# Kernel optimization log

Hardware: AMD Instinct MI355X
Metric: run time of the kernel (lower is better)

The kernel has to match this reference:

```python
import jax, jax.numpy as jnp
import numpy as np

N_NODES = 100_000
N_EDGES = 1_600_000
D = 128
BN_EPS = 1e-5
GIN_EPS = 0.0  # GINConv default eps, train_eps=False


def setup_inputs() -> dict:
    key = jax.random.key(0)
    ks = jax.random.split(key, 8)
    x = jax.random.normal(ks[0], (N_NODES, D), dtype=jnp.float32)
    edge_index = jax.random.randint(ks[1], (2, N_EDGES), 0, N_NODES, dtype=jnp.int64)
    s = 1.0 / np.sqrt(D)
    W1 = jax.random.uniform(ks[2], (D, D), jnp.float32, -s, s)
    b1 = jax.random.uniform(ks[3], (D,), jnp.float32, -s, s)
    W2 = jax.random.uniform(ks[4], (D, D), jnp.float32, -s, s)
    b2 = jax.random.uniform(ks[5], (D,), jnp.float32, -s, s)
    W3 = jax.random.uniform(ks[6], (D, D), jnp.float32, -s, s)
    g1 = jnp.ones((D,), jnp.float32)
    be1 = jnp.zeros((D,), jnp.float32)
    g2 = jnp.ones((D,), jnp.float32)
    be2 = jnp.zeros((D,), jnp.float32)
    return {"x": x, "edge_index": edge_index,
            "W1": W1, "b1": b1, "g1": g1, "be1": be1,
            "W2": W2, "b2": b2, "g2": g2, "be2": be2,
            "W3": W3}


def _batchnorm(h, gamma, beta):
    # training-mode BatchNorm1d over node dim with biased variance
    mean = jnp.mean(h, axis=0)
    var = jnp.mean(jnp.square(h - mean), axis=0)
    return (h - mean) * jax.lax.rsqrt(var + BN_EPS) * gamma + beta


def reference(x, edge_index, W1, b1, g1, be1, W2, b2, g2, be2, W3):
    src, dst = edge_index[0], edge_index[1]
    # GIN aggregation: (1+eps)*x_i + sum_{j->i} x_j  (scatter-add over edges)
    agg = jax.ops.segment_sum(x[src], dst, num_segments=N_NODES)
    h = (1.0 + GIN_EPS) * x + agg
    # MLP: Linear+BN+ReLU x2, then Linear (no bias)
    h = jax.nn.relu(_batchnorm(h @ W1.T + b1, g1, be1))
    h = jax.nn.relu(_batchnorm(h @ W2.T + b2, g2, be2))
    h = h @ W3.T
    # GINLayer final activation (bn=None)
    return jax.nn.relu(h)
```

## Files before the change

### kernel.cpp

```cpp
#include <hip/hip_runtime.h>

#define NN 100000
#define NE 1600000
#define DD 128
#define NCB 196
#define TILE 2048
#define NTILE 782
#define TILEC 4096
#define NTILEC 391
#define FCAP 12288
#define SREP 32
#define WPAD 17408
#define GROWS 256

typedef __attribute__((ext_vector_type(8))) short bf16x8;
typedef __attribute__((ext_vector_type(4))) float f32x4;

union u4bf8 { uint4 u; bf16x8 v; };

__device__ __forceinline__ ushort f2bf(float f) {
    union { float f; uint i; } v; v.f = f;
    uint i = v.i;
    return (ushort)((i + 0x7fffu + ((i >> 16) & 1u)) >> 16);
}
__device__ __forceinline__ float bf2f(ushort u) {
    union { uint i; float f; } v; v.i = ((uint)u) << 16; return v.f;
}
__device__ __forceinline__ float blo(uint v) { return bf2f((ushort)(v & 0xffffu)); }
__device__ __forceinline__ float bhi(uint v) { return bf2f((ushort)(v >> 16)); }

__global__ __launch_bounds__(256) void k_xbh(const float* __restrict__ x,
                                             uint* __restrict__ xb,
                                             const int* __restrict__ ei,
                                             int* __restrict__ ghistP,
                                             const float* __restrict__ W1,
                                             const float* __restrict__ W2,
                                             const float* __restrict__ W3,
                                             ushort* __restrict__ Wbp) {
    __shared__ int h[NCB];
    int t = threadIdx.x;
    if (t < NCB) h[t] = 0;
    __syncthreads();
    int base = blockIdx.x * TILE;
#pragma unroll
    for (int i = 0; i < 8; ++i) {
        int e = base + i * 256 + t;
        if (e < NE) atomicAdd(&h[ei[NE + e] >> 9], 1);
    }
    int gid = blockIdx.x * 256 + t;
#pragma unroll
    for (int i = 0; i < 8; ++i) {
        int item = i * (NTILE * 256) + gid;
        if (item < NN * 16) {
            int n = item >> 4, q = item & 15;
            const float* xp = x + (size_t)n * DD + q * 8;
            float4 a = *(const float4*)xp;
            float4 b = *(const float4*)(xp + 4);
            uint4 pk;
            pk.x = (uint)f2bf(a.x) | ((uint)f2bf(a.y) << 16);
            pk.y = (uint)f2bf(a.z) | ((uint)f2bf(a.w) << 16);
            pk.z = (uint)f2bf(b.x) | ((uint)f2bf(b.y) << 16);
            pk.w = (uint)f2bf(b.z) | ((uint)f2bf(b.w) << 16);
            *(uint4*)(xb + (size_t)n * 64 + q * 4) = pk;
        }
    }
    int c = gid;
    if (c < 6144) {
        int l = c >> 11;
        int cc = c & 2047;
        int r = cc >> 4, c8 = (cc & 15) * 8;
        const float* Wl = (l == 0) ? W1 : (l == 1) ? W2 : W3;
        const float* p = Wl + r * DD + c8;
        float4 a = *(const float4*)p;
        float4 b = *(const float4*)(p + 4);
        uint4 pk;
        pk.x = (uint)f2bf(a.x) | ((uint)f2bf(a.y) << 16);
        pk.y = (uint)f2bf(a.z) | ((uint)f2bf(a.w) << 16);
        pk.z = (uint)f2bf(b.x) | ((uint)f2bf(b.y) << 16);
        pk.w = (uint)f2bf(b.z) | ((uint)f2bf(b.w) << 16);
        *(uint4*)&Wbp[(size_t)l * WPAD + r * 136 + c8] = pk;
    }
    __syncthreads();
    if (t < NCB && h[t] > 0) atomicAdd(&ghistP[t * 16], h[t]);
}

__global__ __launch_bounds__(256) void k_cscatter(const int* __restrict__ ei,
                                                  const int* __restrict__ ghistP,
                                                  int* __restrict__ gcurP,
                                                  uint* __restrict__ buck) {
    __shared__ int h[NCB];
    __shared__ int tb[NCB];
    __shared__ int sh[256];
    int t = threadIdx.x;
    if (t < NCB) h[t] = 0;
    __syncthreads();
    int base = blockIdx.x * TILEC;
    uint vv[16]; int bb[16]; int rr[16];
#pragma unroll
    for (int i = 0; i < 16; ++i) {
        int e = base + i * 256 + t;
        bb[i] = -1;
        if (e < NE) {
            int s = ei[e], d = ei[NE + e];
            int b = d >> 9;
            bb[i] = b;
            vv[i] = (uint)s | ((uint)(d & 511) << 17);
            rr[i] = atomicAdd(&h[b], 1);
        }
    }
    __syncthreads();
    int my = (t < NCB) ? ghistP[t * 16] : 0;
    sh[t] = my;
    __syncthreads();
    for (int o = 1; o < 256; o <<= 1) {
        int u = (t >= o) ? sh[t - o] : 0;
        __syncthreads();
        sh[t] += u;
        __syncthreads();
    }
    if (t < NCB && h[t] > 0)
        tb[t] = (sh[t] - my) + atomicAdd(&gcurP[t * 16], h[t]);
    __syncthreads();
#pragma unroll
    for (int i = 0; i < 16; ++i) {
        if (bb[i] >= 0) buck[tb[bb[i]] + rr[i]] = vv[i];
    }
}

__global__ __launch_bounds__(256) void k_fsort(const uint* __restrict__ buck,
                                               const int* __restrict__ ghistP,
                                               int* __restrict__ csr,
                                               int* __restrict__ rowp) {
    __shared__ uint ebuf[FCAP];
    __shared__ int cnt[512];
    __shared__ int sd[256];
    __shared__ int sh[256];
    int c = blockIdx.x, t = threadIdx.x;
    cnt[t] = 0; cnt[t + 256] = 0;
    int my = (t < NCB) ? ghistP[t * 16] : 0;
    sh[t] = my;
    __syncthreads();
    for (int o = 1; o < 256; o <<= 1) {
        int u = (t >= o) ? sh[t - o] : 0;
        __syncthreads();
        sh[t] += u;
        __syncthreads();
    }
    int s1 = sh[c];
    int hc = ghistP[c * 16];
    int s0 = s1 - hc;
    int len = hc;
    int cap = (len < FCAP) ? len : FCAP;
    for (int i = t; i < cap; i += 256) ebuf[i] = buck[s0 + i];
    __syncthreads();
    for (int i = t; i < len; i += 256) {
        uint v = (i < FCAP) ? ebuf[i] : buck[s0 + i];
        atomicAdd(&cnt[(v >> 17) & 511], 1);
    }
    __syncthreads();
    int p = cnt[2 * t], q = cnt[2 * t + 1];
    sd[t] = p + q;
    __syncthreads();
    for (int o = 1; o < 256; o <<= 1) {
        int u = (t >= o) ? sd[t - o] : 0;
        __syncthreads();
        sd[t] += u;
        __syncthreads();
    }
    int base = sd[t] - (p + q);
    rowp[c * 512 + 2 * t]     = s0 + base;
    rowp[c * 512 + 2 * t + 1] = s0 + base + p;
    __syncthreads();
    cnt[2 * t] = base;
    cnt[2 * t + 1] = base + p;
    __syncthreads();
    for (int i = t; i < len; i += 256) {
        uint v = (i < FCAP) ? ebuf[i] : buck[s0 + i];
        int ld = (int)((v >> 17) & 511u);
        int pos = atomicAdd(&cnt[ld], 1);
        csr[s0 + pos] = (int)(v & 0x1FFFFu);
    }
}

#define B8(ACC0, ACC1, SJ, J)                                               \
    {                                                                       \
        int s0 = __shfl(SJ, J),     s1 = __shfl(SJ, J + 1);                 \
        int s2 = __shfl(SJ, J + 2), s3 = __shfl(SJ, J + 3);                 \
        int s4 = __shfl(SJ, J + 4), s5 = __shfl(SJ, J + 5);                 \
        int s6 = __shfl(SJ, J + 6), s7 = __shfl(SJ, J + 7);                 \
        uint v0 = xb[(size_t)s0 * 64 + lane], v1 = xb[(size_t)s1 * 64 + lane]; \
        uint v2 = xb[(size_t)s2 * 64 + lane], v3 = xb[(size_t)s3 * 64 + lane]; \
        uint v4 = xb[(size_t)s4 * 64 + lane], v5 = xb[(size_t)s5 * 64 + lane]; \
        uint v6 = xb[(size_t)s6 * 64 + lane], v7 = xb[(size_t)s7 * 64 + lane]; \
        ACC0 += blo(v0) + blo(v1) + blo(v2) + blo(v3)                       \
              + blo(v4) + blo(v5) + blo(v6) + blo(v7);                      \
        ACC1 += bhi(v0) + bhi(v1) + bhi(v2) + bhi(v3)                       \
              + bhi(v4) + bhi(v5) + bhi(v6) + bhi(v7);                      \
    }

__global__ __launch_bounds__(256) void k_gather(const uint* __restrict__ xb,
                                                const int* __restrict__ rowp,
                                                const int* __restrict__ csr,
                                                ushort* __restrict__ agg) {
    const int HALF = NN / 2;
    int wave = threadIdx.x >> 6, lane = threadIdx.x & 63;
    int w = blockIdx.x * 4 + wave;
    if (w >= HALF) return;
    int nA = w, nB = w + HALF;
    uint sA = xb[(size_t)nA * 64 + lane];
    uint sB = xb[(size_t)nB * 64 + lane];
    float a0 = blo(sA), a1 = bhi(sA);
    float b0 = blo(sB), b1 = bhi(sB);
    int iA = rowp[nA], eA = rowp[nA + 1];
    int iB = rowp[nB], eB = rowp[nB + 1];

    while (iA < eA || iB < eB) {
        int mA = eA - iA; if (mA > 64) mA = 64; if (mA < 0) mA = 0;
        int mB = eB - iB; if (mB > 64) mB = 64; if (mB < 0) mB = 0;
        int sjA = (lane < mA) ? csr[iA + lane] : 0;
        int sjB = (lane < mB) ? csr[iB + lane] : 0;
        int j = 0, k = 0;
        while (j + 8 <= mA && k + 8 <= mB) {
            int t0 = __shfl(sjA, j),     t1 = __shfl(sjA, j + 1);
            int t2 = __shfl(sjA, j + 2), t3 = __shfl(sjA, j + 3);
            int t4 = __shfl(sjA, j + 4), t5 = __shfl(sjA, j + 5);
            int t6 = __shfl(sjA, j + 6), t7 = __shfl(sjA, j + 7);
            int u0 = __shfl(sjB, k),     u1 = __shfl(sjB, k + 1);
            int u2 = __shfl(sjB, k + 2), u3 = __shfl(sjB, k + 3);
            int u4 = __shfl(sjB, k + 4), u5 = __shfl(sjB, k + 5);
            int u6 = __shfl(sjB, k + 6), u7 = __shfl(sjB, k + 7);
            uint vA0 = xb[(size_t)t0 * 64 + lane], vA1 = xb[(size_t)t1 * 64 + lane];
            uint vA2 = xb[(size_t)t2 * 64 + lane], vA3 = xb[(size_t)t3 * 64 + lane];
            uint vA4 = xb[(size_t)t4 * 64 + lane], vA5 = xb[(size_t)t5 * 64 + lane];
            uint vA6 = xb[(size_t)t6 * 64 + lane], vA7 = xb[(size_t)t7 * 64 + lane];
            uint vB0 = xb[(size_t)u0 * 64 + lane], vB1 = xb[(size_t)u1 * 64 + lane];
            uint vB2 = xb[(size_t)u2 * 64 + lane], vB3 = xb[(size_t)u3 * 64 + lane];
            uint vB4 = xb[(size_t)u4 * 64 + lane], vB5 = xb[(size_t)u5 * 64 + lane];
            uint vB6 = xb[(size_t)u6 * 64 + lane], vB7 = xb[(size_t)u7 * 64 + lane];
            a0 += blo(vA0) + blo(vA1) + blo(vA2) + blo(vA3)
                + blo(vA4) + blo(vA5) + blo(vA6) + blo(vA7);
            a1 += bhi(vA0) + bhi(vA1) + bhi(vA2) + bhi(vA3)
                + bhi(vA4) + bhi(vA5) + bhi(vA6) + bhi(vA7);
            b0 += blo(vB0) + blo(vB1) + blo(vB2) + blo(vB3)
                + blo(vB4) + blo(vB5) + blo(vB6) + blo(vB7);
            b1 += bhi(vB0) + bhi(vB1) + bhi(vB2) + bhi(vB3)
                + bhi(vB4) + bhi(vB5) + bhi(vB6) + bhi(vB7);
            j += 8; k += 8;
        }
        while (j + 8 <= mA) { B8(a0, a1, sjA, j) j += 8; }
        while (k + 8 <= mB) { B8(b0, b1, sjB, k) k += 8; }
        while (j < mA && k < mB) {
            int t = __shfl(sjA, j); int u = __shfl(sjB, k);
            uint vA = xb[(size_t)t * 64 + lane];
            uint vB = xb[(size_t)u * 64 + lane];
            a0 += blo(vA); a1 += bhi(vA);
            b0 += blo(vB); b1 += bhi(vB);
            ++j; ++k;
        }
        while (j < mA) {
            int t = __shfl(sjA, j++);
            uint vA = xb[(size_t)t * 64 + lane];
            a0 += blo(vA); a1 += bhi(vA);
        }
        while (k < mB) {
            int u = __shfl(sjB, k++);
            uint vB = xb[(size_t)u * 64 + lane];
            b0 += blo(vB); b1 += bhi(vB);
        }
        iA += mA; iB += mB;
    }

    uint pkA = (uint)f2bf(a0) | ((uint)f2bf(a1) << 16);
    uint pkB = (uint)f2bf(b0) | ((uint)f2bf(b1) << 16);
    ((uint*)(agg + (size_t)nA * DD))[lane] = pkA;
    ((uint*)(agg + (size_t)nB * DD))[lane] = pkB;
}

template <int MODE>
__global__ __launch_bounds__(256) void k_gemm(const ushort* __restrict__ Ain,
                                              const ushort* __restrict__ Wp,
                                              const float* __restrict__ bias,
                                              const float* __restrict__ statsIn,
                                              const float* __restrict__ g,
                                              const float* __restrict__ be,
                                              void* __restrict__ Outv,
                                              float* __restrict__ statsOut) {
    __shared__ __align__(16) ushort lw[DD * 136];
    __shared__ float red[2][4][DD];
    __shared__ float lac[2 * DD];

    int tid = threadIdx.x;
    int wave = tid >> 6, lane = tid & 63;
    int lm = lane & 15, quad = lane >> 4;

    int row00 = blockIdx.x * GROWS + wave * 16;
    int ar0 = (row00 + lm < NN) ? row00 + lm : 0;
    uint4 araw[4];
#pragma unroll
    for (int kb = 0; kb < 4; ++kb) {
        araw[kb] = *(const uint4*)(Ain + (size_t)ar0 * DD + kb * 32 + quad * 8);
    }

#pragma unroll
    for (int it = 0; it < 8; ++it) {
        int o8 = (it * 256 + tid) * 8;
        *(uint4*)&lw[o8] = *(const uint4*)&Wp[o8];
    }
    if (tid < 128) {
        int o8 = 16384 + tid * 8;
        *(uint4*)&lw[o8] = *(const uint4*)&Wp[o8];
    }
    if constexpr (MODE != 1) {
        if (tid < DD) {
            float S = 0.f, Q = 0.f;
#pragma unroll
            for (int r = 0; r < SREP; ++r) {
                S += statsIn[(r << 8) + tid];
                Q += statsIn[(r << 8) + DD + tid];
            }
            float inv = 1.f / (float)NN;
            float mean = S * inv;
            float var = Q * inv - mean * mean;
            float a = g[tid] * rsqrtf(var + 1e-5f);
            lac[tid] = a;
            lac[DD + tid] = be[tid] - mean * a;
        }
    }
    __syncthreads();

    ushort* Out16 = (ushort*)Outv;
    float* Out32 = (float*)Outv;

    float csum[8], csq[8];
#pragma unroll
    for (int nt = 0; nt < 8; ++nt) { csum[nt] = 0.f; csq[nt] = 0.f; }

#pragma unroll
    for (int sub = 0; sub < 4; ++sub) {
        int row0 = blockIdx.x * GROWS + sub * 64 + wave * 16;
        int arow = row0 + lm;
        int ar = (arow < NN) ? arow : 0;

        bf16x8 afrag[4];
#pragma unroll
        for (int kb = 0; kb < 4; ++kb) {
            int k0 = kb * 32 + quad * 8;
            u4bf8 u;
            if (sub == 0) u.u = araw[kb];
            else          u.u = *(const uint4*)(Ain + (size_t)ar * DD + k0);
            if constexpr (MODE == 1) {
                afrag[kb] = u.v;
            } else {
                uint pk[4] = {u.u.x, u.u.y, u.u.z, u.u.w};
                bf16x8 af;
#pragma unroll
                for (int jj = 0; jj < 4; ++jj) {
                    int k = k0 + jj * 2;
                    float v0 = blo(pk[jj]);
                    float v1 = bhi(pk[jj]);
                    v0 = fmaxf(fmaf(v0, lac[k], lac[DD + k]), 0.f);
                    v1 = fmaxf(fmaf(v1, lac[k + 1], lac[DD + k + 1]), 0.f);
                    af[jj * 2]     = (short)f2bf(v0);
                    af[jj * 2 + 1] = (short)f2bf(v1);
                }
                afrag[kb] = af;
            }
        }

        f32x4 acc[8];
#pragma unroll
        for (int nt = 0; nt < 8; ++nt) {
            float bv = (MODE == 3) ? 0.f : bias[nt * 16 + lm];
            acc[nt] = (f32x4){bv, bv, bv, bv};
        }

#pragma unroll
        for (int kb = 0; kb < 4; ++kb) {
#pragma unroll
            for (int nt = 0; nt < 8; ++nt) {
                bf16x8 bfrag = *(const bf16x8*)&lw[(nt * 16 + lm) * 136 + kb * 32 + quad * 8];
                acc[nt] = __builtin_amdgcn_mfma_f32_16x16x32_bf16(afrag[kb], bfrag, acc[nt], 0, 0, 0);
            }
        }

#pragma unroll
        for (int nt = 0; nt < 8; ++nt) {
            int col = nt * 16 + lm;
#pragma unroll
            for (int r = 0; r < 4; ++r) {
                int row = row0 + quad * 4 + r;
                float v = acc[nt][r];
                if (MODE == 3) v = fmaxf(v, 0.f);
                if (row < NN) {
                    if constexpr (MODE == 3) Out32[(size_t)row * DD + col] = v;
                    else Out16[(size_t)row * DD + col] = f2bf(v);
                    csum[nt] += v;
                    csq[nt] += v * v;
                }
            }
        }
    }

    if constexpr (MODE != 3) {
#pragma unroll
        for (int nt = 0; nt < 8; ++nt) {
            float s = csum[nt], q = csq[nt];
            s += __shfl_down(s, 16, 64); q += __shfl_down(q, 16, 64);
            s += __shfl_down(s, 32, 64); q += __shfl_down(q, 32, 64);
            if (quad == 0) {
                red[0][wave][nt * 16 + lm] = s;
                red[1][wave][nt * 16 + lm] = q;
            }
        }
        __syncthreads();
        if (tid < DD) {
            float S = red[0][0][tid] + red[0][1][tid] + red[0][2][tid] + red[0][3][tid];
            float Q = red[1][0][tid] + red[1][1][tid] + red[1][2][tid] + red[1][3][tid];
            int rep = (blockIdx.x & (SREP - 1)) << 8;
            atomicAdd(&statsOut[rep + tid], S);
            atomicAdd(&statsOut[rep + DD + tid], Q);
        }
    }
}

extern "C" void kernel_launch(void* const* d_in, const int* in_sizes, int n_in,
                              void* d_out, int out_size, void* d_ws, size_t ws_size,
                              hipStream_t stream) {
    const float* x   = (const float*)d_in[0];
    const int* ei    = (const int*)d_in[1];
    const float* W1  = (const float*)d_in[2];
    const float* b1  = (const float*)d_in[3];
    const float* g1  = (const float*)d_in[4];
    const float* be1 = (const float*)d_in[5];
    const float* W2  = (const float*)d_in[6];
    const float* b2  = (const float*)d_in[7];
    const float* g2  = (const float*)d_in[8];
    const float* be2 = (const float*)d_in[9];
    const float* W3  = (const float*)d_in[10];

    float* stats  = (float*)d_ws;
    float* stats2 = stats + SREP * 256;
    int* ghistP   = (int*)(stats2 + SREP * 256);
    int* gcurP    = ghistP + NCB * 16;
    ushort* Wbp   = (ushort*)(gcurP + NCB * 16);
    int* rowp     = (int*)(Wbp + 3 * WPAD);
    uint* buck    = (uint*)(rowp + NCB * 512 + 4);
    int* csr      = (int*)(buck + NE);
    ushort* agg   = (ushort*)(((uintptr_t)(csr + NE) + 15) & ~(uintptr_t)15);
    uint* xb     = (uint*)d_out;
    ushort* t1   = (ushort*)d_out + (size_t)NN * DD;
    ushort* t2   = agg;
    float* outp  = (float*)d_out;

    int gblk = (NN + GROWS - 1) / GROWS;
    hipMemsetAsync(stats, 0, (2 * SREP * 256) * sizeof(float) + 2 * NCB * 16 * sizeof(int), stream);
    k_xbh<<<NTILE, 256, 0, stream>>>(x, xb, ei, ghistP, W1, W2, W3, Wbp);
    k_cscatter<<<NTILEC, 256, 0, stream>>>(ei, ghistP, gcurP, buck);
    k_fsort<<<NCB, 256, 0, stream>>>(buck, ghistP, csr, rowp);
    k_gather<<<(NN / 2 + 3) / 4, 256, 0, stream>>>(xb, rowp, csr, agg);
    k_gemm<1><<<gblk, 256, 0, stream>>>(agg, Wbp, b1, nullptr, nullptr, nullptr, t1, stats);
    k_gemm<2><<<gblk, 256, 0, stream>>>(t1, Wbp + WPAD, b2, stats, g1, be1, t2, stats2);
    k_gemm<3><<<gblk, 256, 0, stream>>>(t2, Wbp + 2 * WPAD, nullptr, stats2, g2, be2, outp, nullptr);
}
```

Before: 292.9 us.

## Fuse gather and three GEMM stages into one cooperative persistent kernel

Merges the neighbor-gather kernel and the three MFMA GEMM/BatchNorm stages into a single cooperative kernel. The stages are separated by grid-wide syncs, and the grid is sized from the occupancy query, capped at four blocks per CU. Each stage uses grid-stride loops over its work items. This is meant to remove the launch and drain gaps between the four back-to-back kernels. In exchange it adds grid-sync overhead and caps the gather phase's wave count, which can hurt a latency-bound gather. It also ties the gather phase to the GEMM's LDS footprint.

```diff
diff --git a/kernel.cpp b/kernel.cpp
--- a/kernel.cpp
+++ b/kernel.cpp
@@ -1,4 +1,7 @@
 #include <hip/hip_runtime.h>
+#include <hip/hip_cooperative_groups.h>
+
+namespace cg = cooperative_groups;
 
 #define NN 100000
 #define NE 1600000
@@ -12,6 +15,7 @@
 #define SREP 32
 #define WPAD 17408
 #define GROWS 256
+#define GBLK 391
 
 typedef __attribute__((ext_vector_type(8))) short bf16x8;
 typedef __attribute__((ext_vector_type(4))) float f32x4;
@@ -198,229 +202,254 @@
               + bhi(v4) + bhi(v5) + bhi(v6) + bhi(v7);                      \
     }
 
-__global__ __launch_bounds__(256) void k_gather(const uint* __restrict__ xb,
-                                                const int* __restrict__ rowp,
-                                                const int* __restrict__ csr,
-                                                ushort* __restrict__ agg) {
-    const int HALF = NN / 2;
-    int wave = threadIdx.x >> 6, lane = threadIdx.x & 63;
-    int w = blockIdx.x * 4 + wave;
-    if (w >= HALF) return;
-    int nA = w, nB = w + HALF;
-    uint sA = xb[(size_t)nA * 64 + lane];
-    uint sB = xb[(size_t)nB * 64 + lane];
-    float a0 = blo(sA), a1 = bhi(sA);
-    float b0 = blo(sB), b1 = bhi(sB);
-    int iA = rowp[nA], eA = rowp[nA + 1];
-    int iB = rowp[nB], eB = rowp[nB + 1];
-
-    while (iA < eA || iB < eB) {
-        int mA = eA - iA; if (mA > 64) mA = 64; if (mA < 0) mA = 0;
-        int mB = eB - iB; if (mB > 64) mB = 64; if (mB < 0) mB = 0;
-        int sjA = (lane < mA) ? csr[iA + lane] : 0;
-        int sjB = (lane < mB) ? csr[iB + lane] : 0;
-        int j = 0, k = 0;
-        while (j + 8 <= mA && k + 8 <= mB) {
-            int t0 = __shfl(sjA, j),     t1 = __shfl(sjA, j + 1);
-            int t2 = __shfl(sjA, j + 2), t3 = __shfl(sjA, j + 3);
-            int t4 = __shfl(sjA, j + 4), t5 = __shfl(sjA, j + 5);
-            int t6 = __shfl(sjA, j + 6), t7 = __shfl(sjA, j + 7);
-            int u0 = __shfl(sjB, k),     u1 = __shfl(sjB, k + 1);
-            int u2 = __shfl(sjB, k + 2), u3 = __shfl(sjB, k + 3);
-            int u4 = __shfl(sjB, k + 4), u5 = __shfl(sjB, k + 5);
-            int u6 = __shfl(sjB, k + 6), u7 = __shfl(sjB, k + 7);
-            uint vA0 = xb[(size_t)t0 * 64 + lane], vA1 = xb[(size_t)t1 * 64 + lane];
-            uint vA2 = xb[(size_t)t2 * 64 + lane], vA3 = xb[(size_t)t3 * 64 + lane];
-            uint vA4 = xb[(size_t)t4 * 64 + lane], vA5 = xb[(size_t)t5 * 64 + lane];
-            uint vA6 = xb[(size_t)t6 * 64 + lane], vA7 = xb[(size_t)t7 * 64 + lane];
-            uint vB0 = xb[(size_t)u0 * 64 + lane], vB1 = xb[(size_t)u1 * 64 + lane];
-            uint vB2 = xb[(size_t)u2 * 64 + lane], vB3 = xb[(size_t)u3 * 64 + lane];
-            uint vB4 = xb[(size_t)u4 * 64 + lane], vB5 = xb[(size_t)u5 * 64 + lane];
-            uint vB6 = xb[(size_t)u6 * 64 + lane], vB7 = xb[(size_t)u7 * 64 + lane];
-            a0 += blo(vA0) + blo(vA1) + blo(vA2) + blo(vA3)
-                + blo(vA4) + blo(vA5) + blo(vA6) + blo(vA7);
-            a1 += bhi(vA0) + bhi(vA1) + bhi(vA2) + bhi(vA3)
-                + bhi(vA4) + bhi(vA5) + bhi(vA6) + bhi(vA7);
-            b0 += blo(vB0) + blo(vB1) + blo(vB2) + blo(vB3)
-                + blo(vB4) + blo(vB5) + blo(vB6) + blo(vB7);
-            b1 += bhi(vB0) + bhi(vB1) + bhi(vB2) + bhi(vB3)
-                + bhi(vB4) + bhi(vB5) + bhi(vB6) + bhi(vB7);
-            j += 8; k += 8;
-        }
-        while (j + 8 <= mA) { B8(a0, a1, sjA, j) j += 8; }
-        while (k + 8 <= mB) { B8(b0, b1, sjB, k) k += 8; }
-        while (j < mA && k < mB) {
-            int t = __shfl(sjA, j); int u = __shfl(sjB, k);
-            uint vA = xb[(size_t)t * 64 + lane];
-            uint vB = xb[(size_t)u * 64 + lane];
-            a0 += blo(vA); a1 += bhi(vA);
-            b0 += blo(vB); b1 += bhi(vB);
-            ++j; ++k;
-        }
-        while (j < mA) {
-            int t = __shfl(sjA, j++);
-            uint vA = xb[(size_t)t * 64 + lane];
-            a0 += blo(vA); a1 += bhi(vA);
-        }
-        while (k < mB) {
-            int u = __shfl(sjB, k++);
-            uint vB = xb[(size_t)u * 64 + lane];
-            b0 += blo(vB); b1 += bhi(vB);
-        }
-        iA += mA; iB += mB;
-    }
-
-    uint pkA = (uint)f2bf(a0) | ((uint)f2bf(a1) << 16);
-    uint pkB = (uint)f2bf(b0) | ((uint)f2bf(b1) << 16);
-    ((uint*)(agg + (size_t)nA * DD))[lane] = pkA;
-    ((uint*)(agg + (size_t)nB * DD))[lane] = pkB;
-}
-
 template <int MODE>
-__global__ __launch_bounds__(256) void k_gemm(const ushort* __restrict__ Ain,
-                                              const ushort* __restrict__ Wp,
-                                              const float* __restrict__ bias,
-                                              const float* __restrict__ statsIn,
-                                              const float* __restrict__ g,
-                                              const float* __restrict__ be,
-                                              void* __restrict__ Outv,
-                                              float* __restrict__ statsOut) {
+__device__ void gemm_phase(const ushort* __restrict__ Ain,
+                           const ushort* __restrict__ Wp,
+                           const float* __restrict__ bias,
+                           const float* __restrict__ statsIn,
+                           const float* __restrict__ g,
+                           const float* __restrict__ be,
+                           void* __restrict__ Outv,
+                           float* __restrict__ statsOut,
+                           ushort* lw, float (*red)[4][DD], float* lac) {
+    int tid = threadIdx.x;
+    int wave = tid >> 6, lane = tid & 63;
+    int lm = lane & 15, quad = lane >> 4;
+    ushort* Out16 = (ushort*)Outv;
+    float* Out32 = (float*)Outv;
+
+    for (int tile = blockIdx.x; tile < GBLK; tile += gridDim.x) {
+        int row00 = tile * GROWS + wave * 16;
+        int ar0 = (row00 + lm < NN) ? row00 + lm : 0;
+        uint4 araw[4];
+#pragma unroll
+        for (int kb = 0; kb < 4; ++kb)
+            araw[kb] = *(const uint4*)(Ain + (size_t)ar0 * DD + kb * 32 + quad * 8);
+
+#pragma unroll
+        for (int it = 0; it < 8; ++it) {
+            int o8 = (it * 256 + tid) * 8;
+            *(uint4*)&lw[o8] = *(const uint4*)&Wp[o8];
+        }
+        if (tid < 128) {
+            int o8 = 16384 + tid * 8;
+            *(uint4*)&lw[o8] = *(const uint4*)&Wp[o8];
+        }
+        if constexpr (MODE != 1) {
+            if (tid < DD) {
+                float S = 0.f, Q = 0.f;
+#pragma unroll
+                for (int r = 0; r < SREP; ++r) {
+                    S += statsIn[(r << 8) + tid];
+                    Q += statsIn[(r << 8) + DD + tid];
+                }
+                float inv = 1.f / (float)NN;
+                float mean = S * inv;
+                float var = Q * inv - mean * mean;
+                float a = g[tid] * rsqrtf(var + 1e-5f);
+                lac[tid] = a;
+                lac[DD + tid] = be[tid] - mean * a;
+            }
+        }
+        __syncthreads();
+
+        float csum[8], csq[8];
+#pragma unroll
+        for (int nt = 0; nt < 8; ++nt) { csum[nt] = 0.f; csq[nt] = 0.f; }
+
+#pragma unroll
+        for (int sub = 0; sub < 4; ++sub) {
+            int row0 = tile * GROWS + sub * 64 + wave * 16;
+            int arow = row0 + lm;
+            int ar = (arow < NN) ? arow : 0;
+
+            bf16x8 afrag[4];
+#pragma unroll
+            for (int kb = 0; kb < 4; ++kb) {
+                int k0 = kb * 32 + quad * 8;
+                u4bf8 u;
+                if (sub == 0) u.u = araw[kb];
+                else          u.u = *(const uint4*)(Ain + (size_t)ar * DD + k0);
+                if constexpr (MODE == 1) {
+                    afrag[kb] = u.v;
+                } else {
+                    uint pk[4] = {u.u.x, u.u.y, u.u.z, u.u.w};
+                    bf16x8 af;
+#pragma unroll
+                    for (int jj = 0; jj < 4; ++jj) {
+                        int k = k0 + jj * 2;
+                        float v0 = blo(pk[jj]);
+                        float v1 = bhi(pk[jj]);
+                        v0 = fmaxf(fmaf(v0, lac[k], lac[DD + k]), 0.f);
+                        v1 = fmaxf(fmaf(v1, lac[k + 1], lac[DD + k + 1]), 0.f);
+                        af[jj * 2]     = (short)f2bf(v0);
+                        af[jj * 2 + 1] = (short)f2bf(v1);
+                    }
+                    afrag[kb] = af;
+                }
+            }
+
+            f32x4 acc[8];
+#pragma unroll
+            for (int nt = 0; nt < 8; ++nt) {
+                float bv = (MODE == 3) ? 0.f : bias[nt * 16 + lm];
+                acc[nt] = (f32x4){bv, bv, bv, bv};
+            }
+
+#pragma unroll
+            for (int kb = 0; kb < 4; ++kb) {
+#pragma unroll
+                for (int nt = 0; nt < 8; ++nt) {
+                    bf16x8 bfrag = *(const bf16x8*)&lw[(nt * 16 + lm) * 136 + kb * 32 + quad * 8];
+                    acc[nt] = __builtin_amdgcn_mfma_f32_16x16x32_bf16(afrag[kb], bfrag, acc[nt], 0, 0, 0);
+                }
+            }
+
+#pragma unroll
+            for (int nt = 0; nt < 8; ++nt) {
+                int col = nt * 16 + lm;
+#pragma unroll
+                for (int r = 0; r < 4; ++r) {
+                    int row = row0 + quad * 4 + r;
+                    float v = acc[nt][r];
+                    if (MODE == 3) v = fmaxf(v, 0.f);
+                    if (row < NN) {
+                        if constexpr (MODE == 3) Out32[(size_t)row * DD + col] = v;
+                        else Out16[(size_t)row * DD + col] = f2bf(v);
+                        csum[nt] += v;
+                        csq[nt] += v * v;
+                    }
+                }
+            }
+        }
+
+        if constexpr (MODE != 3) {
+#pragma unroll
+            for (int nt = 0; nt < 8; ++nt) {
+                float s = csum[nt], q = csq[nt];
+                s += __shfl_down(s, 16, 64); q += __shfl_down(q, 16, 64);
+                s += __shfl_down(s, 32, 64); q += __shfl_down(q, 32, 64);
+                if (quad == 0) {
+                    red[0][wave][nt * 16 + lm] = s;
+                    red[1][wave][nt * 16 + lm] = q;
+                }
+            }
+            __syncthreads();
+            if (tid < DD) {
+                float S = red[0][0][tid] + red[0][1][tid] + red[0][2][tid] + red[0][3][tid];
+                float Q = red[1][0][tid] + red[1][1][tid] + red[1][2][tid] + red[1][3][tid];
+                int rep = (tile & (SREP - 1)) << 8;
+                atomicAdd(&statsOut[rep + tid], S);
+                atomicAdd(&statsOut[rep + DD + tid], Q);
+            }
+        }
+        __syncthreads();
+    }
+}
+
+struct TailArgs {
+    const uint* xb; const int* rowp; const int* csr; ushort* agg;
+    const ushort* Wbp;
+    const float* b1; const float* b2;
+    const float* g1; const float* be1; const float* g2; const float* be2;
+    ushort* t1; ushort* t2; float* outp;
+    float* stats; float* stats2;
+};
+
+__global__ __launch_bounds__(256, 4) void k_tail(TailArgs a) {
     __shared__ __align__(16) ushort lw[DD * 136];
     __shared__ float red[2][4][DD];
     __shared__ float lac[2 * DD];
-
-    int tid = threadIdx.x;
-    int wave = tid >> 6, lane = tid & 63;
-    int lm = lane & 15, quad = lane >> 4;
-
-    int row00 = blockIdx.x * GROWS + wave * 16;
-    int ar0 = (row00 + lm < NN) ? row00 + lm : 0;
-    uint4 araw[4];
-#pragma unroll
-    for (int kb = 0; kb < 4; ++kb) {
-        araw[kb] = *(const uint4*)(Ain + (size_t)ar0 * DD + kb * 32 + quad * 8);
-    }
-
-#pragma unroll
-    for (int it = 0; it < 8; ++it) {
-        int o8 = (it * 256 + tid) * 8;
-        *(uint4*)&lw[o8] = *(const uint4*)&Wp[o8];
-    }
-    if (tid < 128) {
-        int o8 = 16384 + tid * 8;
-        *(uint4*)&lw[o8] = *(const uint4*)&Wp[o8];
-    }
-    if constexpr (MODE != 1) {
-        if (tid < DD) {
-            float S = 0.f, Q = 0.f;
-#pragma unroll
-            for (int r = 0; r < SREP; ++r) {
-                S += statsIn[(r << 8) + tid];
-                Q += statsIn[(r << 8) + DD + tid];
-            }
-            float inv = 1.f / (float)NN;
-            float mean = S * inv;
-            float var = Q * inv - mean * mean;
-            float a = g[tid] * rsqrtf(var + 1e-5f);
-            lac[tid] = a;
-            lac[DD + tid] = be[tid] - mean * a;
-        }
-    }
-    __syncthreads();
-
-    ushort* Out16 = (ushort*)Outv;
-    float* Out32 = (float*)Outv;
-
-    float csum[8], csq[8];
-#pragma unroll
-    for (int nt = 0; nt < 8; ++nt) { csum[nt] = 0.f; csq[nt] = 0.f; }
-
-#pragma unroll
-    for (int sub = 0; sub < 4; ++sub) {
-        int row0 = blockIdx.x * GROWS + sub * 64 + wave * 16;
-        int arow = row0 + lm;
-        int ar = (arow < NN) ? arow : 0;
-
-        bf16x8 afrag[4];
-#pragma unroll
-        for (int kb = 0; kb < 4; ++kb) {
-            int k0 = kb * 32 + quad * 8;
-            u4bf8 u;
-            if (sub == 0) u.u = araw[kb];
-            else          u.u = *(const uint4*)(Ain + (size_t)ar * DD + k0);
-            if constexpr (MODE == 1) {
-                afrag[kb] = u.v;
-            } else {
-                uint pk[4] = {u.u.x, u.u.y, u.u.z, u.u.w};
-                bf16x8 af;
-#pragma unroll
-                for (int jj = 0; jj < 4; ++jj) {
-                    int k = k0 + jj * 2;
-                    float v0 = blo(pk[jj]);
-                    float v1 = bhi(pk[jj]);
-                    v0 = fmaxf(fmaf(v0, lac[k], lac[DD + k]), 0.f);
-                    v1 = fmaxf(fmaf(v1, lac[k + 1], lac[DD + k + 1]), 0.f);
-                    af[jj * 2]     = (short)f2bf(v0);
-                    af[jj * 2 + 1] = (short)f2bf(v1);
-                }
-                afrag[kb] = af;
-            }
-        }
-
-        f32x4 acc[8];
-#pragma unroll
-        for (int nt = 0; nt < 8; ++nt) {
-            float bv = (MODE == 3) ? 0.f : bias[nt * 16 + lm];
-            acc[nt] = (f32x4){bv, bv, bv, bv};
-        }
-
-#pragma unroll
-        for (int kb = 0; kb < 4; ++kb) {
-#pragma unroll
-            for (int nt = 0; nt < 8; ++nt) {
-                bf16x8 bfrag = *(const bf16x8*)&lw[(nt * 16 + lm) * 136 + kb * 32 + quad * 8];
-                acc[nt] = __builtin_amdgcn_mfma_f32_16x16x32_bf16(afrag[kb], bfrag, acc[nt], 0, 0, 0);
-            }
-        }
-
-#pragma unroll
-        for (int nt = 0; nt < 8; ++nt) {
-            int col = nt * 16 + lm;
-#pragma unroll
-            for (int r = 0; r < 4; ++r) {
-                int row = row0 + quad * 4 + r;
-                float v = acc[nt][r];
-                if (MODE == 3) v = fmaxf(v, 0.f);
-                if (row < NN) {
-                    if constexpr (MODE == 3) Out32[(size_t)row * DD + col] = v;
-                    else Out16[(size_t)row * DD + col] = f2bf(v);
-                    csum[nt] += v;
-                    csq[nt] += v * v;
-                }
-            }
-        }
-    }
-
-    if constexpr (MODE != 3) {
-#pragma unroll
-        for (int nt = 0; nt < 8; ++nt) {
-            float s = csum[nt], q = csq[nt];
-            s += __shfl_down(s, 16, 64); q += __shfl_down(q, 16, 64);
-            s += __shfl_down(s, 32, 64); q += __shfl_down(q, 32, 64);
-            if (quad == 0) {
-                red[0][wave][nt * 16 + lm] = s;
-                red[1][wave][nt * 16 + lm] = q;
-            }
-        }
-        __syncthreads();
-        if (tid < DD) {
-            float S = red[0][0][tid] + red[0][1][tid] + red[0][2][tid] + red[0][3][tid];
-            float Q = red[1][0][tid] + red[1][1][tid] + red[1][2][tid] + red[1][3][tid];
-            int rep = (blockIdx.x & (SREP - 1)) << 8;
-            atomicAdd(&statsOut[rep + tid], S);
-            atomicAdd(&statsOut[rep + DD + tid], Q);
-        }
-    }
+    cg::grid_group grid = cg::this_grid();
+
+    {
+        const uint* __restrict__ xb = a.xb;
+        const int* __restrict__ rowp = a.rowp;
+        const int* __restrict__ csr = a.csr;
+        ushort* __restrict__ agg = a.agg;
+        const int HALF = NN / 2;
+        int wave = threadIdx.x >> 6, lane = threadIdx.x & 63;
+        int wstep = gridDim.x * 4;
+        for (int w = blockIdx.x * 4 + wave; w < HALF; w += wstep) {
+            int nA = w, nB = w + HALF;
+            uint sA = xb[(size_t)nA * 64 + lane];
+            uint sB = xb[(size_t)nB * 64 + lane];
+            float a0 = blo(sA), a1 = bhi(sA);
+            float b0 = blo(sB), b1 = bhi(sB);
+            int iA = rowp[nA], eA = rowp[nA + 1];
+            int iB = rowp[nB], eB = rowp[nB + 1];
+
+            while (iA < eA || iB < eB) {
+                int mA = eA - iA; if (mA > 64) mA = 64; if (mA < 0) mA = 0;
+                int mB = eB - iB; if (mB > 64) mB = 64; if (mB < 0) mB = 0;
+                int sjA = (lane < mA) ? csr[iA + lane] : 0;
+                int sjB = (lane < mB) ? csr[iB + lane] : 0;
+                int j = 0, k = 0;
+                while (j + 8 <= mA && k + 8 <= mB) {
+                    int t0 = __shfl(sjA, j),     t1 = __shfl(sjA, j + 1);
+                    int t2 = __shfl(sjA, j + 2), t3 = __shfl(sjA, j + 3);
+                    int t4 = __shfl(sjA, j + 4), t5 = __shfl(sjA, j + 5);
+                    int t6 = __shfl(sjA, j + 6), t7 = __shfl(sjA, j + 7);
+                    int u0 = __shfl(sjB, k),     u1 = __shfl(sjB, k + 1);
+                    int u2 = __shfl(sjB, k + 2), u3 = __shfl(sjB, k + 3);
+                    int u4 = __shfl(sjB, k + 4), u5 = __shfl(sjB, k + 5);
+                    int u6 = __shfl(sjB, k + 6), u7 = __shfl(sjB, k + 7);
+                    uint vA0 = xb[(size_t)t0 * 64 + lane], vA1 = xb[(size_t)t1 * 64 + lane];
+                    uint vA2 = xb[(size_t)t2 * 64 + lane], vA3 = xb[(size_t)t3 * 64 + lane];
+                    uint vA4 = xb[(size_t)t4 * 64 + lane], vA5 = xb[(size_t)t5 * 64 + lane];
+                    uint vA6 = xb[(size_t)t6 * 64 + lane], vA7 = xb[(size_t)t7 * 64 + lane];
+                    uint vB0 = xb[(size_t)u0 * 64 + lane], vB1 = xb[(size_t)u1 * 64 + lane];
+                    uint vB2 = xb[(size_t)u2 * 64 + lane], vB3 = xb[(size_t)u3 * 64 + lane];
+                    uint vB4 = xb[(size_t)u4 * 64 + lane], vB5 = xb[(size_t)u5 * 64 + lane];
+                    uint vB6 = xb[(size_t)u6 * 64 + lane], vB7 = xb[(size_t)u7 * 64 + lane];
+                    a0 += blo(vA0) + blo(vA1) + blo(vA2) + blo(vA3)
+                        + blo(vA4) + blo(vA5) + blo(vA6) + blo(vA7);
+                    a1 += bhi(vA0) + bhi(vA1) + bhi(vA2) + bhi(vA3)
+                        + bhi(vA4) + bhi(vA5) + bhi(vA6) + bhi(vA7);
+                    b0 += blo(vB0) + blo(vB1) + blo(vB2) + blo(vB3)
+                        + blo(vB4) + blo(vB5) + blo(vB6) + blo(vB7);
+                    b1 += bhi(vB0) + bhi(vB1) + bhi(vB2) + bhi(vB3)
+                        + bhi(vB4) + bhi(vB5) + bhi(vB6) + bhi(vB7);
+                    j += 8; k += 8;
+                }
+                while (j + 8 <= mA) { B8(a0, a1, sjA, j) j += 8; }
+                while (k + 8 <= mB) { B8(b0, b1, sjB, k) k += 8; }
+                while (j < mA && k < mB) {
+                    int t = __shfl(sjA, j); int u = __shfl(sjB, k);
+                    uint vA = xb[(size_t)t * 64 + lane];
+                    uint vB = xb[(size_t)u * 64 + lane];
+                    a0 += blo(vA); a1 += bhi(vA);
+                    b0 += blo(vB); b1 += bhi(vB);
+                    ++j; ++k;
+                }
+                while (j < mA) {
+                    int t = __shfl(sjA, j++);
+                    uint vA = xb[(size_t)t * 64 + lane];
+                    a0 += blo(vA); a1 += bhi(vA);
+                }
+                while (k < mB) {
+                    int u = __shfl(sjB, k++);
+                    uint vB = xb[(size_t)u * 64 + lane];
+                    b0 += blo(vB); b1 += bhi(vB);
+                }
+                iA += mA; iB += mB;
+            }
+
+            uint pkA = (uint)f2bf(a0) | ((uint)f2bf(a1) << 16);
+            uint pkB = (uint)f2bf(b0) | ((uint)f2bf(b1) << 16);
+            ((uint*)(agg + (size_t)nA * DD))[lane] = pkA;
+            ((uint*)(agg + (size_t)nB * DD))[lane] = pkB;
+        }
+    }
+    __threadfence();
+    grid.sync();
+    gemm_phase<1>(a.agg, a.Wbp, a.b1, nullptr, nullptr, nullptr, a.t1, a.stats, lw, red, lac);
+    __threadfence();
+    grid.sync();
+    gemm_phase<2>(a.t1, a.Wbp + WPAD, a.b2, a.stats, a.g1, a.be1, a.t2, a.stats2, lw, red, lac);
+    __threadfence();
+    grid.sync();
+    gemm_phase<3>(a.t2, a.Wbp + 2 * WPAD, nullptr, a.stats2, a.g2, a.be2, a.outp, nullptr, lw, red, lac);
 }
 
 extern "C" void kernel_launch(void* const* d_in, const int* in_sizes, int n_in,
@@ -452,13 +481,28 @@
     ushort* t2   = agg;
     float* outp  = (float*)d_out;
 
-    int gblk = (NN + GROWS - 1) / GROWS;
+    static int gblocks = 0;
+    if (gblocks == 0) {
+        int nb = 0;
+        hipOccupancyMaxActiveBlocksPerMultiprocessor(&nb, k_tail, 256, 0);
+        if (nb < 1) nb = 1;
+        if (nb > 4) nb = 4;
+        gblocks = nb * 256;
+    }
+
     hipMemsetAsync(stats, 0, (2 * SREP * 256) * sizeof(float) + 2 * NCB * 16 * sizeof(int), stream);
     k_xbh<<<NTILE, 256, 0, stream>>>(x, xb, ei, ghistP, W1, W2, W3, Wbp);
     k_cscatter<<<NTILEC, 256, 0, stream>>>(ei, ghistP, gcurP, buck);
     k_fsort<<<NCB, 256, 0, stream>>>(buck, ghistP, csr, rowp);
-    k_gather<<<(NN / 2 + 3) / 4, 256, 0, stream>>>(xb, rowp, csr, agg);
-    k_gemm<1><<<gblk, 256, 0, stream>>>(agg, Wbp, b1, nullptr, nullptr, nullptr, t1, stats);
-    k_gemm<2><<<gblk, 256, 0, stream>>>(t1, Wbp + WPAD, b2, stats, g1, be1, t2, stats2);
-    k_gemm<3><<<gblk, 256, 0, stream>>>(t2, Wbp + 2 * WPAD, nullptr, stats2, g2, be2, outp, nullptr);
-}
+
+    TailArgs ha;
+    ha.xb = xb; ha.rowp = rowp; ha.csr = csr; ha.agg = agg;
+    ha.Wbp = Wbp;
+    ha.b1 = b1; ha.b2 = b2;
+    ha.g1 = g1; ha.be1 = be1; ha.g2 = g2; ha.be2 = be2;
+    ha.t1 = t1; ha.t2 = t2; ha.outp = outp;
+    ha.stats = stats; ha.stats2 = stats2;
+    void* kargs[] = { (void*)&ha };
+    hipLaunchCooperativeKernel((const void*)k_tail, dim3(gblocks), dim3(256),
+                               kargs, 0, stream);
+}
```

Measured after the change: 901.4 us. 208% more time.

## Fuse neighbor gather with first GEMM and BN stats into one kernel

Applied to the files above, without the earlier changes.

Replaces the separate gather kernel and the first GEMM with a single kernel. Each block aggregates 64 nodes (each wave handles 16 nodes, two at a time), writes them to agg, then loads W1 into LDS and runs the MFMA GEMM on those rows, accumulating BN statistics. This removes one kernel launch and keeps the freshly written agg rows likely in cache for the GEMM. In exchange, each block reloads W1 into LDS for only 64 rows, and the gather's node pairing becomes local instead of spread across halves of the graph, which may hurt load balance and occupancy because of the large LDS footprint.

```diff
diff --git a/kernel.cpp b/kernel.cpp
--- a/kernel.cpp
+++ b/kernel.cpp
@@ -198,82 +198,174 @@
               + bhi(v4) + bhi(v5) + bhi(v6) + bhi(v7);                      \
     }
 
-__global__ __launch_bounds__(256) void k_gather(const uint* __restrict__ xb,
-                                                const int* __restrict__ rowp,
-                                                const int* __restrict__ csr,
-                                                ushort* __restrict__ agg) {
-    const int HALF = NN / 2;
-    int wave = threadIdx.x >> 6, lane = threadIdx.x & 63;
-    int w = blockIdx.x * 4 + wave;
-    if (w >= HALF) return;
-    int nA = w, nB = w + HALF;
-    uint sA = xb[(size_t)nA * 64 + lane];
-    uint sB = xb[(size_t)nB * 64 + lane];
-    float a0 = blo(sA), a1 = bhi(sA);
-    float b0 = blo(sB), b1 = bhi(sB);
-    int iA = rowp[nA], eA = rowp[nA + 1];
-    int iB = rowp[nB], eB = rowp[nB + 1];
-
-    while (iA < eA || iB < eB) {
-        int mA = eA - iA; if (mA > 64) mA = 64; if (mA < 0) mA = 0;
-        int mB = eB - iB; if (mB > 64) mB = 64; if (mB < 0) mB = 0;
-        int sjA = (lane < mA) ? csr[iA + lane] : 0;
-        int sjB = (lane < mB) ? csr[iB + lane] : 0;
-        int j = 0, k = 0;
-        while (j + 8 <= mA && k + 8 <= mB) {
-            int t0 = __shfl(sjA, j),     t1 = __shfl(sjA, j + 1);
-            int t2 = __shfl(sjA, j + 2), t3 = __shfl(sjA, j + 3);
-            int t4 = __shfl(sjA, j + 4), t5 = __shfl(sjA, j + 5);
-            int t6 = __shfl(sjA, j + 6), t7 = __shfl(sjA, j + 7);
-            int u0 = __shfl(sjB, k),     u1 = __shfl(sjB, k + 1);
-            int u2 = __shfl(sjB, k + 2), u3 = __shfl(sjB, k + 3);
-            int u4 = __shfl(sjB, k + 4), u5 = __shfl(sjB, k + 5);
-            int u6 = __shfl(sjB, k + 6), u7 = __shfl(sjB, k + 7);
-            uint vA0 = xb[(size_t)t0 * 64 + lane], vA1 = xb[(size_t)t1 * 64 + lane];
-            uint vA2 = xb[(size_t)t2 * 64 + lane], vA3 = xb[(size_t)t3 * 64 + lane];
-            uint vA4 = xb[(size_t)t4 * 64 + lane], vA5 = xb[(size_t)t5 * 64 + lane];
-            uint vA6 = xb[(size_t)t6 * 64 + lane], vA7 = xb[(size_t)t7 * 64 + lane];
-            uint vB0 = xb[(size_t)u0 * 64 + lane], vB1 = xb[(size_t)u1 * 64 + lane];
-            uint vB2 = xb[(size_t)u2 * 64 + lane], vB3 = xb[(size_t)u3 * 64 + lane];
-            uint vB4 = xb[(size_t)u4 * 64 + lane], vB5 = xb[(size_t)u5 * 64 + lane];
-            uint vB6 = xb[(size_t)u6 * 64 + lane], vB7 = xb[(size_t)u7 * 64 + lane];
-            a0 += blo(vA0) + blo(vA1) + blo(vA2) + blo(vA3)
-                + blo(vA4) + blo(vA5) + blo(vA6) + blo(vA7);
-            a1 += bhi(vA0) + bhi(vA1) + bhi(vA2) + bhi(vA3)
-                + bhi(vA4) + bhi(vA5) + bhi(vA6) + bhi(vA7);
-            b0 += blo(vB0) + blo(vB1) + blo(vB2) + blo(vB3)
-                + blo(vB4) + blo(vB5) + blo(vB6) + blo(vB7);
-            b1 += bhi(vB0) + bhi(vB1) + bhi(vB2) + bhi(vB3)
-                + bhi(vB4) + bhi(vB5) + bhi(vB6) + bhi(vB7);
-            j += 8; k += 8;
-        }
-        while (j + 8 <= mA) { B8(a0, a1, sjA, j) j += 8; }
-        while (k + 8 <= mB) { B8(b0, b1, sjB, k) k += 8; }
-        while (j < mA && k < mB) {
-            int t = __shfl(sjA, j); int u = __shfl(sjB, k);
-            uint vA = xb[(size_t)t * 64 + lane];
-            uint vB = xb[(size_t)u * 64 + lane];
-            a0 += blo(vA); a1 += bhi(vA);
-            b0 += blo(vB); b1 += bhi(vB);
-            ++j; ++k;
-        }
-        while (j < mA) {
-            int t = __shfl(sjA, j++);
-            uint vA = xb[(size_t)t * 64 + lane];
-            a0 += blo(vA); a1 += bhi(vA);
-        }
-        while (k < mB) {
-            int u = __shfl(sjB, k++);
-            uint vB = xb[(size_t)u * 64 + lane];
-            b0 += blo(vB); b1 += bhi(vB);
-        }
-        iA += mA; iB += mB;
-    }
-
-    uint pkA = (uint)f2bf(a0) | ((uint)f2bf(a1) << 16);
-    uint pkB = (uint)f2bf(b0) | ((uint)f2bf(b1) << 16);
-    ((uint*)(agg + (size_t)nA * DD))[lane] = pkA;
-    ((uint*)(agg + (size_t)nB * DD))[lane] = pkB;
+__global__ __launch_bounds__(256) void k_gg1(const uint* __restrict__ xb,
+                                             const int* __restrict__ rowp,
+                                             const int* __restrict__ csr,
+                                             ushort* __restrict__ agg,
+                                             const ushort* __restrict__ Wp,
+                                             const float* __restrict__ bias,
+                                             ushort* __restrict__ Out16,
+                                             float* __restrict__ statsOut) {
+    __shared__ __align__(16) ushort lw[DD * 136];
+    __shared__ float red[2][4][DD];
+    int tid = threadIdx.x, wave = tid >> 6, lane = tid & 63;
+
+    int nbase = blockIdx.x * 64 + wave * 16;
+    for (int i = 0; i < 8; ++i) {
+        int nA = nbase + i, nB = nbase + i + 8;
+        if (nA >= NN) break;
+        bool okB = (nB < NN);
+        uint sA = xb[(size_t)nA * 64 + lane];
+        float a0 = blo(sA), a1 = bhi(sA);
+        float b0 = 0.f, b1 = 0.f;
+        int iA = rowp[nA], eA = rowp[nA + 1];
+        int iB = 0, eB = 0;
+        if (okB) {
+            uint sB = xb[(size_t)nB * 64 + lane];
+            b0 = blo(sB); b1 = bhi(sB);
+            iB = rowp[nB]; eB = rowp[nB + 1];
+        }
+
+        while (iA < eA || iB < eB) {
+            int mA = eA - iA; if (mA > 64) mA = 64; if (mA < 0) mA = 0;
+            int mB = eB - iB; if (mB > 64) mB = 64; if (mB < 0) mB = 0;
+            int sjA = (lane < mA) ? csr[iA + lane] : 0;
+            int sjB = (lane < mB) ? csr[iB + lane] : 0;
+            int j = 0, k = 0;
+            while (j + 8 <= mA && k + 8 <= mB) {
+                int t0 = __shfl(sjA, j),     t1 = __shfl(sjA, j + 1);
+                int t2 = __shfl(sjA, j + 2), t3 = __shfl(sjA, j + 3);
+                int t4 = __shfl(sjA, j + 4), t5 = __shfl(sjA, j + 5);
+                int t6 = __shfl(sjA, j + 6), t7 = __shfl(sjA, j + 7);
+                int u0 = __shfl(sjB, k),     u1 = __shfl(sjB, k + 1);
+                int u2 = __shfl(sjB, k + 2), u3 = __shfl(sjB, k + 3);
+                int u4 = __shfl(sjB, k + 4), u5 = __shfl(sjB, k + 5);
+                int u6 = __shfl(sjB, k + 6), u7 = __shfl(sjB, k + 7);
+                uint vA0 = xb[(size_t)t0 * 64 + lane], vA1 = xb[(size_t)t1 * 64 + lane];
+                uint vA2 = xb[(size_t)t2 * 64 + lane], vA3 = xb[(size_t)t3 * 64 + lane];
+                uint vA4 = xb[(size_t)t4 * 64 + lane], vA5 = xb[(size_t)t5 * 64 + lane];
+                uint vA6 = xb[(size_t)t6 * 64 + lane], vA7 = xb[(size_t)t7 * 64 + lane];
+                uint vB0 = xb[(size_t)u0 * 64 + lane], vB1 = xb[(size_t)u1 * 64 + lane];
+                uint vB2 = xb[(size_t)u2 * 64 + lane], vB3 = xb[(size_t)u3 * 64 + lane];
+                uint vB4 = xb[(size_t)u4 * 64 + lane], vB5 = xb[(size_t)u5 * 64 + lane];
+                uint vB6 = xb[(size_t)u6 * 64 + lane], vB7 = xb[(size_t)u7 * 64 + lane];
+                a0 += blo(vA0) + blo(vA1) + blo(vA2) + blo(vA3)
+                    + blo(vA4) + blo(vA5) + blo(vA6) + blo(vA7);
+                a1 += bhi(vA0) + bhi(vA1) + bhi(vA2) + bhi(vA3)
+                    + bhi(vA4) + bhi(vA5) + bhi(vA6) + bhi(vA7);
+                b0 += blo(vB0) + blo(vB1) + blo(vB2) + blo(vB3)
+                    + blo(vB4) + blo(vB5) + blo(vB6) + blo(vB7);
+                b1 += bhi(vB0) + bhi(vB1) + bhi(vB2) + bhi(vB3)
+                    + bhi(vB4) + bhi(vB5) + bhi(vB6) + bhi(vB7);
+                j += 8; k += 8;
+            }
+            while (j + 8 <= mA) { B8(a0, a1, sjA, j) j += 8; }
+            while (k + 8 <= mB) { B8(b0, b1, sjB, k) k += 8; }
+            while (j < mA && k < mB) {
+                int t = __shfl(sjA, j); int u = __shfl(sjB, k);
+                uint vA = xb[(size_t)t * 64 + lane];
+                uint vB = xb[(size_t)u * 64 + lane];
+                a0 += blo(vA); a1 += bhi(vA);
+                b0 += blo(vB); b1 += bhi(vB);
+                ++j; ++k;
+            }
+            while (j < mA) {
+                int t = __shfl(sjA, j++);
+                uint vA = xb[(size_t)t * 64 + lane];
+                a0 += blo(vA); a1 += bhi(vA);
+            }
+            while (k < mB) {
+                int u = __shfl(sjB, k++);
+                uint vB = xb[(size_t)u * 64 + lane];
+                b0 += blo(vB); b1 += bhi(vB);
+            }
+            iA += mA; iB += mB;
+        }
+
+        uint pkA = (uint)f2bf(a0) | ((uint)f2bf(a1) << 16);
+        ((uint*)(agg + (size_t)nA * DD))[lane] = pkA;
+        if (okB) {
+            uint pkB = (uint)f2bf(b0) | ((uint)f2bf(b1) << 16);
+            ((uint*)(agg + (size_t)nB * DD))[lane] = pkB;
+        }
+    }
+
+#pragma unroll
+    for (int it = 0; it < 8; ++it) {
+        int o8 = (it * 256 + tid) * 8;
+        *(uint4*)&lw[o8] = *(const uint4*)&Wp[o8];
+    }
+    if (tid < 128) {
+        int o8 = 16384 + tid * 8;
+        *(uint4*)&lw[o8] = *(const uint4*)&Wp[o8];
+    }
+    __syncthreads();
+
+    int lm = lane & 15, quad = lane >> 4;
+    int row0 = blockIdx.x * 64 + wave * 16;
+    int arow = row0 + lm;
+    int ar = (arow < NN) ? arow : 0;
+
+    bf16x8 afrag[4];
+#pragma unroll
+    for (int kb = 0; kb < 4; ++kb) {
+        u4bf8 u;
+        u.u = *(const uint4*)(agg + (size_t)ar * DD + kb * 32 + quad * 8);
+        afrag[kb] = u.v;
+    }
+
+    f32x4 acc[8];
+#pragma unroll
+    for (int nt = 0; nt < 8; ++nt) {
+        float bv = bias[nt * 16 + lm];
+        acc[nt] = (f32x4){bv, bv, bv, bv};
+    }
+
+#pragma unroll
+    for (int kb = 0; kb < 4; ++kb) {
+#pragma unroll
+        for (int nt = 0; nt < 8; ++nt) {
+            bf16x8 bfrag = *(const bf16x8*)&lw[(nt * 16 + lm) * 136 + kb * 32 + quad * 8];
+            acc[nt] = __builtin_amdgcn_mfma_f32_16x16x32_bf16(afrag[kb], bfrag, acc[nt], 0, 0, 0);
+        }
+    }
+
+    float csum[8], csq[8];
+#pragma unroll
+    for (int nt = 0; nt < 8; ++nt) {
+        int col = nt * 16 + lm;
+        float s = 0.f, q = 0.f;
+#pragma unroll
+        for (int r = 0; r < 4; ++r) {
+            int row = row0 + quad * 4 + r;
+            float v = acc[nt][r];
+            if (row < NN) {
+                Out16[(size_t)row * DD + col] = f2bf(v);
+                s += v;
+                q += v * v;
+            }
+        }
+        csum[nt] = s; csq[nt] = q;
+    }
+
+#pragma unroll
+    for (int nt = 0; nt < 8; ++nt) {
+        float s = csum[nt], q = csq[nt];
+        s += __shfl_down(s, 16, 64); q += __shfl_down(q, 16, 64);
+        s += __shfl_down(s, 32, 64); q += __shfl_down(q, 32, 64);
+        if (quad == 0) {
+            red[0][wave][nt * 16 + lm] = s;
+            red[1][wave][nt * 16 + lm] = q;
+        }
+    }
+    __syncthreads();
+    if (tid < DD) {
+        float S = red[0][0][tid] + red[0][1][tid] + red[0][2][tid] + red[0][3][tid];
+        float Q = red[1][0][tid] + red[1][1][tid] + red[1][2][tid] + red[1][3][tid];
+        int rep = (blockIdx.x & (SREP - 1)) << 8;
+        atomicAdd(&statsOut[rep + tid], S);
+        atomicAdd(&statsOut[rep + DD + tid], Q);
+    }
 }
 
 template <int MODE>
@@ -310,21 +402,19 @@
         int o8 = 16384 + tid * 8;
         *(uint4*)&lw[o8] = *(const uint4*)&Wp[o8];
     }
-    if constexpr (MODE != 1) {
-        if (tid < DD) {
-            float S = 0.f, Q = 0.f;
-#pragma unroll
-            for (int r = 0; r < SREP; ++r) {
-                S += statsIn[(r << 8) + tid];
-                Q += statsIn[(r << 8) + DD + tid];
-            }
-            float inv = 1.f / (float)NN;
-            float mean = S * inv;
-            float var = Q * inv - mean * mean;
-            float a = g[tid] * rsqrtf(var + 1e-5f);
-            lac[tid] = a;
-            lac[DD + tid] = be[tid] - mean * a;
-        }
+    if (tid < DD) {
+        float S = 0.f, Q = 0.f;
+#pragma unroll
+        for (int r = 0; r < SREP; ++r) {
+            S += statsIn[(r << 8) + tid];
+            Q += statsIn[(r << 8) + DD + tid];
+        }
+        float inv = 1.f / (float)NN;
+        float mean = S * inv;
+        float var = Q * inv - mean * mean;
+        float a = g[tid] * rsqrtf(var + 1e-5f);
+        lac[tid] = a;
+        lac[DD + tid] = be[tid] - mean * a;
     }
     __syncthreads();
 
@@ -348,23 +438,19 @@
             u4bf8 u;
             if (sub == 0) u.u = araw[kb];
             else          u.u = *(const uint4*)(Ain + (size_t)ar * DD + k0);
-            if constexpr (MODE == 1) {
-                afrag[kb] = u.v;
-            } else {
-                uint pk[4] = {u.u.x, u.u.y, u.u.z, u.u.w};
-                bf16x8 af;
-#pragma unroll
-                for (int jj = 0; jj < 4; ++jj) {
-                    int k = k0 + jj * 2;
-                    float v0 = blo(pk[jj]);
-                    float v1 = bhi(pk[jj]);
-                    v0 = fmaxf(fmaf(v0, lac[k], lac[DD + k]), 0.f);
-                    v1 = fmaxf(fmaf(v1, lac[k + 1], lac[DD + k + 1]), 0.f);
-                    af[jj * 2]     = (short)f2bf(v0);
-                    af[jj * 2 + 1] = (short)f2bf(v1);
-                }
-                afrag[kb] = af;
-            }
+            uint pk[4] = {u.u.x, u.u.y, u.u.z, u.u.w};
+            bf16x8 af;
+#pragma unroll
+            for (int jj = 0; jj < 4; ++jj) {
+                int k = k0 + jj * 2;
+                float v0 = blo(pk[jj]);
+                float v1 = bhi(pk[jj]);
+                v0 = fmaxf(fmaf(v0, lac[k], lac[DD + k]), 0.f);
+                v1 = fmaxf(fmaf(v1, lac[k + 1], lac[DD + k + 1]), 0.f);
+                af[jj * 2]     = (short)f2bf(v0);
+                af[jj * 2 + 1] = (short)f2bf(v1);
+            }
+            afrag[kb] = af;
         }
 
         f32x4 acc[8];
@@ -452,13 +538,13 @@
     ushort* t2   = agg;
     float* outp  = (float*)d_out;
 
-    int gblk = (NN + GROWS - 1) / GROWS;
+    int g1blk = (NN + 63) / 64;
+    int gblk  = (NN + GROWS - 1) / GROWS;
     hipMemsetAsync(stats, 0, (2 * SREP * 256) * sizeof(float) + 2 * NCB * 16 * sizeof(int), stream);
     k_xbh<<<NTILE, 256, 0, stream>>>(x, xb, ei, ghistP, W1, W2, W3, Wbp);
     k_cscatter<<<NTILEC, 256, 0, stream>>>(ei, ghistP, gcurP, buck);
     k_fsort<<<NCB, 256, 0, stream>>>(buck, ghistP, csr, rowp);
-    k_gather<<<(NN / 2 + 3) / 4, 256, 0, stream>>>(xb, rowp, csr, agg);
-    k_gemm<1><<<gblk, 256, 0, stream>>>(agg, Wbp, b1, nullptr, nullptr, nullptr, t1, stats);
+    k_gg1<<<g1blk, 256, 0, stream>>>(xb, rowp, csr, agg, Wbp, b1, t1, stats);
     k_gemm<2><<<gblk, 256, 0, stream>>>(t1, Wbp + WPAD, b2, stats, g1, be1, t2, stats2);
     k_gemm<3><<<gblk, 256, 0, stream>>>(t2, Wbp + 2 * WPAD, nullptr, stats2, g2, be2, outp, nullptr);
 }
```

After: 357.6 us. 1.22x slower.
